# Performance work log

Measured on AMD Instinct MI355X. Metric: run time of the kernel, lower is better.

Reference implementation:

```python
import jax, jax.numpy as jnp
import numpy as np

HIDDEN = 1024
N_HEADS = 16
HEAD_DIM = HIDDEN // N_HEADS


def apply_rope(x, freqs):
    # x: [b, s, h, d]; freqs: [s, d//2]
    b, s, h, d = x.shape
    x2 = x.reshape(b, s, h, d // 2, 2)
    x_real, x_imag = x2[..., 0], x2[..., 1]
    cos = jnp.cos(freqs)[None, :, None, :]  # [1, s, 1, d//2]
    sin = jnp.sin(freqs)[None, :, None, :]
    out_real = x_real * cos - x_imag * sin
    out_imag = x_real * sin + x_imag * cos
    return jnp.stack([out_real, out_imag], axis=-1).reshape(b, s, h, d)


def setup_inputs() -> dict:
    key = jax.random.key(0)
    k_x, k_f, k_wq, k_bq, k_wo, k_bo = jax.random.split(key, 6)
    b, s = 2, 2048
    x = jax.random.normal(k_x, (b, s, HIDDEN), dtype=jnp.float32)
    freqs = jax.random.normal(k_f, (s, HEAD_DIM // 2), dtype=jnp.float32)
    lim = 1.0 / np.sqrt(HIDDEN)
    W_qkv = jax.random.uniform(k_wq, (HIDDEN, 3 * HIDDEN), jnp.float32, -lim, lim)
    b_qkv = jax.random.uniform(k_bq, (3 * HIDDEN,), jnp.float32, -lim, lim)
    W_out = jax.random.uniform(k_wo, (HIDDEN, HIDDEN), jnp.float32, -lim, lim)
    b_out = jax.random.uniform(k_bo, (HIDDEN,), jnp.float32, -lim, lim)
    return {"x": x, "freqs": freqs, "W_qkv": W_qkv, "b_qkv": b_qkv,
            "W_out": W_out, "b_out": b_out}


def reference(x, freqs, W_qkv, b_qkv, W_out, b_out):
    b, s, c = x.shape
    h, d = N_HEADS, HEAD_DIM
    qkv = jnp.einsum('bsc,cf->bsf', x, W_qkv) + b_qkv  # [b, s, 3*c]
    qkv = qkv.reshape(b, s, 3, h, d)
    q, k, v = qkv[:, :, 0], qkv[:, :, 1], qkv[:, :, 2]  # [b, s, h, d]
    q = apply_rope(q, freqs)
    k = apply_rope(k, freqs)
    scale = 1.0 / np.sqrt(d).astype(np.float32)
    scores = jnp.einsum('bqhd,bkhd->bhqk', q, k) * scale  # [b, h, s, s]
    attn = jax.nn.softmax(scores, axis=-1)
    out = jnp.einsum('bhqk,bkhd->bqhd', attn, v).reshape(b, s, c)
    return jnp.einsum('bsc,cf->bsf', out, W_out) + b_out
```

## Files before the change

### kernel.cpp

```cpp
#include <hip/hip_runtime.h>
#include <math.h>

constexpr int kB = 2;
constexpr int kS = 2048;
constexpr int kC = 1024;
constexpr int kH = 16;
constexpr int kD = 64;
constexpr int kF = 3072;
constexpr int kT = kB * kS;

typedef __attribute__((ext_vector_type(8))) short short8v;
typedef __attribute__((ext_vector_type(4))) short short4v;
typedef __attribute__((ext_vector_type(4))) float f32x4;
typedef __attribute__((ext_vector_type(16))) float f32x16;

__device__ __forceinline__ short f2bf(float f) {
    unsigned u = __builtin_bit_cast(unsigned, f);
    u += 0x7fffu + ((u >> 16) & 1u);
    return (short)(u >> 16);
}

__device__ __forceinline__ unsigned cvtpk(float a, float b) {
    unsigned r;
    asm("v_cvt_pk_bf16_f32 %0, %1, %2" : "=v"(r) : "v"(a), "v"(b));
    return r;
}

__device__ __forceinline__ void plane32_swap(unsigned& a, unsigned& b) {
    asm volatile("v_permlane32_swap_b32 %0, %1" : "+v"(a), "+v"(b));
}

__device__ __forceinline__ unsigned pk_bf16(float a, float b) {
    unsigned ua = __builtin_bit_cast(unsigned, a);
    ua += 0x7fffu + ((ua >> 16) & 1u);
    unsigned ub = __builtin_bit_cast(unsigned, b);
    ub += 0x7fffu + ((ub >> 16) & 1u);
    return (ua >> 16) | (ub & 0xffff0000u);
}

__device__ __forceinline__ void gl_lds16(const void* g, void* l) {
    __builtin_amdgcn_global_load_lds(
        (const __attribute__((address_space(1))) char*)g,
        (__attribute__((address_space(3))) char*)l, 16, 0, 0);
}

__device__ __forceinline__ f32x4 mfma16(short8v a, short8v b, f32x4 c) {
    return __builtin_amdgcn_mfma_f32_16x16x32_bf16(a, b, c, 0, 0, 0);
}
__device__ __forceinline__ f32x16 mfma32(short8v a, short8v b, f32x16 c) {
    return __builtin_amdgcn_mfma_f32_32x32x16_bf16(a, b, c, 0, 0, 0);
}

__device__ __forceinline__ void tcvt_body(const float* __restrict__ w,
                                          short* __restrict__ wt, int K, int N,
                                          int bx, int by, int t, float Ts[64][65]) {
    const int n0 = bx * 64, k0 = by * 64;
    const int r = t >> 4, c4 = (t & 15) * 4;
#pragma unroll
    for (int rr = 0; rr < 64; rr += 16) {
        float4 v = *reinterpret_cast<const float4*>(&w[(size_t)(k0 + r + rr) * N + n0 + c4]);
        Ts[r + rr][c4 + 0] = v.x; Ts[r + rr][c4 + 1] = v.y;
        Ts[r + rr][c4 + 2] = v.z; Ts[r + rr][c4 + 3] = v.w;
    }
    __syncthreads();
#pragma unroll
    for (int rr = 0; rr < 64; rr += 16) {
        int n = r + rr;
        short4v o = { f2bf(Ts[c4 + 0][n]), f2bf(Ts[c4 + 1][n]),
                      f2bf(Ts[c4 + 2][n]), f2bf(Ts[c4 + 3][n]) };
        *reinterpret_cast<short4v*>(&wt[(size_t)(n0 + n) * K + k0 + c4]) = o;
    }
}

__global__ __launch_bounds__(256) void prep_kernel(
    const float* __restrict__ x, short* __restrict__ xb,
    const float* __restrict__ wq, short* __restrict__ wqt,
    const float* __restrict__ wo, short* __restrict__ wot,
    const float* __restrict__ freqs, float* __restrict__ cost,
    float* __restrict__ sint) {
    __shared__ float Ts[64][65];
    const int bid = blockIdx.x, t = threadIdx.x;
    if (bid < 4096) {
        int i = bid * 256 + t;
        float4 v = reinterpret_cast<const float4*>(x)[i];
        short4v o = { f2bf(v.x), f2bf(v.y), f2bf(v.z), f2bf(v.w) };
        reinterpret_cast<short4v*>(xb)[i] = o;
    } else if (bid < 4864) {
        int i = bid - 4096;
        tcvt_body(wq, wqt, kC, kF, i % 48, i / 48, t, Ts);
    } else if (bid < 5120) {
        int i = bid - 4864;
        tcvt_body(wo, wot, kC, kC, i % 16, i / 16, t, Ts);
    } else {
        int i = (bid - 5120) * 256 + t;
        float f = freqs[i];
        float s, c;
        sincosf(f, &s, &c);
        cost[i] = c; sint[i] = s;
    }
}

__device__ __forceinline__ void gemm_main(const short* __restrict__ A,
                                          const short* __restrict__ Bt,
                                          int m0, int n0, short* Als, short* Bls,
                                          f32x4 acc[4][4]) {
    const int tid = threadIdx.x, wid = tid >> 6, lane = tid & 63;
    const int srow = lane >> 3, schunk = lane & 7;
    const int fr = lane & 15, fg = lane >> 4;
    const int wm = (wid >> 1) * 64, wn = (wid & 1) * 64;
    for (int kt = 0; kt < 1024; kt += 64) {
        __syncthreads();
#pragma unroll
        for (int j = 0; j < 4; ++j) {
            int i = wid * 4 + j;
            int row = i * 8 + srow;
            gl_lds16(&A[(size_t)(m0 + row) * 1024 + kt + ((schunk ^ (row & 7)) << 3)],
                     &Als[i * 512]);
        }
#pragma unroll
        for (int j = 0; j < 4; ++j) {
            int i = wid * 4 + j;
            int row = i * 8 + srow;
            gl_lds16(&Bt[(size_t)(n0 + row) * 1024 + kt + ((schunk ^ (row & 7)) << 3)],
                     &Bls[i * 512]);
        }
        __syncthreads();
#pragma unroll
        for (int kk = 0; kk < 2; ++kk) {
            short8v af[4], bf[4];
#pragma unroll
            for (int fm = 0; fm < 4; ++fm) {
                int row = wm + fm * 16 + fr;
                af[fm] = *reinterpret_cast<const short8v*>(
                    &Als[row * 64 + (((fg + 4 * kk) ^ (row & 7)) << 3)]);
            }
#pragma unroll
            for (int fn = 0; fn < 4; ++fn) {
                int row = wn + fn * 16 + fr;
                bf[fn] = *reinterpret_cast<const short8v*>(
                    &Bls[row * 64 + (((fg + 4 * kk) ^ (row & 7)) << 3)]);
            }
#pragma unroll
            for (int fm = 0; fm < 4; ++fm)
#pragma unroll
                for (int fn = 0; fn < 4; ++fn)
                    acc[fm][fn] = mfma16(af[fm], bf[fn], acc[fm][fn]);
        }
    }
}

__global__ __launch_bounds__(256) void qkv_gemm_kernel(
    const short* __restrict__ xb, const short* __restrict__ wqt,
    const float* __restrict__ bias, const float* __restrict__ cost,
    const float* __restrict__ sint,
    short* __restrict__ qg, short* __restrict__ kg, short* __restrict__ vt) {
    __shared__ __attribute__((aligned(16))) short Als[128 * 64];
    __shared__ __attribute__((aligned(16))) short Bls[128 * 64];
    f32x4 acc[4][4] = {};
    const int tid = threadIdx.x, wid = tid >> 6, lane = tid & 63;
    const int m0 = blockIdx.y * 128, n0 = blockIdx.x * 128;
    gemm_main(xb, wqt, m0, n0, Als, Bls, acc);

    const int fr = lane & 15, fg = lane >> 4;
    const int wm = (wid >> 1) * 64, wn = (wid & 1) * 64;
    const int which = (n0 + wn) >> 10;
    const int bidx = m0 >> 11;
#pragma unroll
    for (int fn = 0; fn < 4; ++fn) {
        int col = n0 + wn + fn * 16 + fr;
        float bv = bias[col];
        int d = col & 63;
        int h = (col >> 6) & 15;
        int p0 = d >> 1;
        int odd = d & 1;
#pragma unroll
        for (int fm = 0; fm < 4; ++fm) {
            int r0 = m0 + wm + fm * 16 + fg * 4;
            int s0 = r0 & 2047;
            float c[4];
#pragma unroll
            for (int r = 0; r < 4; ++r) c[r] = acc[fm][fn][r] + bv;
            if (which < 2) {
#pragma unroll
                for (int r = 0; r < 4; ++r) {
                    float cs = cost[(s0 + r) * 32 + p0];
                    float sn = sint[(s0 + r) * 32 + p0];
                    float p = __shfl_xor(c[r], 1);
                    float o = odd ? fmaf(p, sn, c[r] * cs) : fmaf(-p, sn, c[r] * cs);
                    c[r] = (which == 0) ? o * 0.1803368801f : o;
                }
                short* dst = which ? kg : qg;
                size_t base = ((size_t)(bidx * 16 + h) * 2048 + s0) * 64 + d;
#pragma unroll
                for (int r = 0; r < 4; ++r) dst[base + (size_t)r * 64] = f2bf(c[r]);
            } else {
                short4v o = { f2bf(c[0]), f2bf(c[1]), f2bf(c[2]), f2bf(c[3]) };
                *reinterpret_cast<short4v*>(
                    &vt[((size_t)(bidx * 16 + h) * 64 + d) * 2048 + s0]) = o;
            }
        }
    }
}

__global__ __launch_bounds__(256, 3) void attn_mfma_kernel(
    const short* __restrict__ qg, const short* __restrict__ kg,
    const short* __restrict__ vt, short* __restrict__ ab) {
    __shared__ __attribute__((aligned(16))) short LDSBUF[16384];
    short* Kls = LDSBUF;
    short* Vls = LDSBUF + 8192;
    const int tid = threadIdx.x, wid = tid >> 6, lane = tid & 63;
    const int l31 = lane & 31, hi = lane >> 5;
    const int r8 = lane >> 3, c8 = lane & 7;

    const int bid = blockIdx.x;
    const int swz = (bid & 7) * 128 + (bid >> 3);
    const int bh = swz >> 5;
    const int q0 = (swz & 31) * 64;

    const short* qb = qg + (size_t)bh * 2048 * 64;
    const short* kb = kg + (size_t)bh * 2048 * 64;
    const short* vb = vt + (size_t)bh * 64 * 2048;

    short8v qf[2][4];
#pragma unroll
    for (int qt = 0; qt < 2; ++qt)
#pragma unroll
        for (int kkq = 0; kkq < 4; ++kkq)
            qf[qt][kkq] = *reinterpret_cast<const short8v*>(
                &qb[(size_t)(q0 + qt * 32 + l31) * 64 + kkq * 16 + hi * 8]);

    f32x16 o[2][2] = {};
    float l_loc[2] = {0.f, 0.f};

    const int soffK = 8 * (c8 ^ r8);

    for (int t = 0; t < 16; ++t) {
        const int kt = t * 128;
        __syncthreads();
#pragma unroll
        for (int j = 0; j < 4; ++j)
            gl_lds16(kb + (size_t)(kt + wid * 32 + j * 8 + r8) * 64 + soffK,
                     Kls + (wid * 32 + j * 8) * 64);
#pragma unroll
        for (int j = 0; j < 4; ++j) {
            int d = wid * 16 + j * 4 + (lane >> 4);
            int c = lane & 15;
            gl_lds16(vb + (size_t)d * 2048 + kt + ((c ^ (d & 15)) * 8),
                     Vls + (wid * 16 + j * 4) * 128);
        }
        __syncthreads();

        f32x16 sacc[2] = {};
#pragma unroll
        for (int kkq = 0; kkq < 4; ++kkq) {
            short8v kf = *reinterpret_cast<const short8v*>(
                &Kls[(wid * 32 + l31) * 64 + (((kkq * 2 + hi) ^ (l31 & 7)) << 3)]);
            sacc[0] = mfma32(kf, qf[0][kkq], sacc[0]);
            sacc[1] = mfma32(kf, qf[1][kkq], sacc[1]);
        }

        short8v pb[2][2];
#pragma unroll
        for (int qt = 0; qt < 2; ++qt) {
#pragma unroll
            for (int r = 0; r < 16; ++r)
                sacc[qt][r] = __builtin_amdgcn_exp2f(sacc[qt][r]);
            float t8[8];
#pragma unroll
            for (int r = 0; r < 8; ++r) t8[r] = sacc[qt][r] + sacc[qt][r + 8];
            float t4[4];
#pragma unroll
            for (int r = 0; r < 4; ++r) t4[r] = t8[r] + t8[r + 4];
            l_loc[qt] += (t4[0] + t4[1]) + (t4[2] + t4[3]);
            unsigned c[4][2];
#pragma unroll
            for (int g = 0; g < 4; ++g) {
                c[g][0] = cvtpk(sacc[qt][g * 4 + 0], sacc[qt][g * 4 + 1]);
                c[g][1] = cvtpk(sacc[qt][g * 4 + 2], sacc[qt][g * 4 + 3]);
            }
#pragma unroll
            for (int kk = 0; kk < 2; ++kk) {
                unsigned x0 = c[2 * kk][0], y0 = c[2 * kk + 1][0];
                unsigned x1 = c[2 * kk][1], y1 = c[2 * kk + 1][1];
                plane32_swap(x0, y0);
                plane32_swap(x1, y1);
                uint4 w;
                w.x = x0; w.y = x1; w.z = y0; w.w = y1;
                pb[qt][kk] = __builtin_bit_cast(short8v, w);
            }
        }

#pragma unroll
        for (int kk = 0; kk < 2; ++kk)
#pragma unroll
            for (int fd = 0; fd < 2; ++fd) {
                int d = fd * 32 + l31;
                short8v vf = *reinterpret_cast<const short8v*>(
                    &Vls[d * 128 + (((wid * 4 + kk * 2 + hi) ^ (d & 15)) << 3)]);
                o[fd][0] = mfma32(vf, pb[0][kk], o[fd][0]);
                o[fd][1] = mfma32(vf, pb[1][kk], o[fd][1]);
            }
    }

    __syncthreads();

    float* Oacc = reinterpret_cast<float*>(LDSBUF);
    float* lacc = Oacc + 64 * 65;
    float l2[2];
#pragma unroll
    for (int qt = 0; qt < 2; ++qt)
        l2[qt] = l_loc[qt] + __shfl_xor(l_loc[qt], 32);
    for (int w = 0; w < 4; ++w) {
        if (wid == w) {
#pragma unroll
            for (int qt = 0; qt < 2; ++qt) {
                int q = qt * 32 + l31;
#pragma unroll
                for (int fd = 0; fd < 2; ++fd)
#pragma unroll
                    for (int r = 0; r < 16; ++r) {
                        int d = fd * 32 + (r & 3) + 8 * (r >> 2) + 4 * hi;
                        if (w == 0) Oacc[q * 65 + d] = o[fd][qt][r];
                        else        Oacc[q * 65 + d] += o[fd][qt][r];
                    }
                if (hi == 0) {
                    if (w == 0) lacc[q] = l2[qt];
                    else        lacc[q] += l2[qt];
                }
            }
        }
        __syncthreads();
    }
    {
        const int q = tid >> 2, dc = (tid & 3) * 16;
        const float inv = 1.f / lacc[q];
        unsigned u[8];
#pragma unroll
        for (int i = 0; i < 8; ++i) {
            float a = Oacc[q * 65 + dc + 2 * i] * inv;
            float b = Oacc[q * 65 + dc + 2 * i + 1] * inv;
            u[i] = pk_bf16(a, b);
        }
        const int bb = bh >> 4, hh = bh & 15;
        size_t base = (size_t)(bb * 2048 + q0 + q) * 1024 + hh * 64 + dc;
        uint4 w0; w0.x = u[0]; w0.y = u[1]; w0.z = u[2]; w0.w = u[3];
        uint4 w1; w1.x = u[4]; w1.y = u[5]; w1.z = u[6]; w1.w = u[7];
        *reinterpret_cast<uint4*>(&ab[base]) = w0;
        *reinterpret_cast<uint4*>(&ab[base + 8]) = w1;
    }
}

__global__ __launch_bounds__(256) void out_gemm_kernel(
    const short* __restrict__ ab, const short* __restrict__ wot,
    const float* __restrict__ bias, float* __restrict__ out) {
    __shared__ __attribute__((aligned(16))) short Als[128 * 64];
    __shared__ __attribute__((aligned(16))) short Bls[128 * 64];
    f32x4 acc[4][4] = {};
    const int tid = threadIdx.x, wid = tid >> 6, lane = tid & 63;
    const int m0 = blockIdx.y * 128, n0 = blockIdx.x * 128;
    gemm_main(ab, wot, m0, n0, Als, Bls, acc);
    const int fr = lane & 15, fg = lane >> 4;
    const int wm = (wid >> 1) * 64, wn = (wid & 1) * 64;
#pragma unroll
    for (int fn = 0; fn < 4; ++fn) {
        int col = n0 + wn + fn * 16 + fr;
        float bv = bias[col];
#pragma unroll
        for (int fm = 0; fm < 4; ++fm) {
            int r0 = m0 + wm + fm * 16 + fg * 4;
#pragma unroll
            for (int r = 0; r < 4; ++r)
                out[(size_t)(r0 + r) * 1024 + col] = acc[fm][fn][r] + bv;
        }
    }
}

extern "C" void kernel_launch(void* const* d_in, const int* in_sizes, int n_in,
                              void* d_out, int out_size, void* d_ws, size_t ws_size,
                              hipStream_t stream) {
    const float* x     = (const float*)d_in[0];
    const float* freqs = (const float*)d_in[1];
    const float* W_qkv = (const float*)d_in[2];
    const float* b_qkv = (const float*)d_in[3];
    const float* W_out = (const float*)d_in[4];
    const float* b_out = (const float*)d_in[5];
    float* out = (float*)d_out;

    char* w = (char*)d_ws;
    short* xb  = (short*)w;  w += (size_t)kT * kC * 2;
    short* wqt = (short*)w;  w += (size_t)kF * kC * 2;
    short* wot = (short*)w;  w += (size_t)kC * kC * 2;
    short* qgw = (short*)w;  w += (size_t)kB * kH * kS * kD * 2;
    short* kgw = (short*)w;  w += (size_t)kB * kH * kS * kD * 2;
    short* vtw = (short*)w;  w += (size_t)kB * kH * kS * kD * 2;
    short* abw = (short*)w;  w += (size_t)kT * kC * 2;
    float* costt = (float*)w; w += (size_t)kS * (kD / 2) * 4;
    float* sintt = (float*)w; w += (size_t)kS * (kD / 2) * 4;

    prep_kernel<<<dim3(5376), 256, 0, stream>>>(x, xb, W_qkv, wqt, W_out, wot,
                                                freqs, costt, sintt);
    qkv_gemm_kernel<<<dim3(kF / 128, kT / 128), 256, 0, stream>>>(
        xb, wqt, b_qkv, costt, sintt, qgw, kgw, vtw);
    attn_mfma_kernel<<<dim3(1024), 256, 0, stream>>>(qgw, kgw, vtw, abw);
    out_gemm_kernel<<<dim3(kC / 128, kT / 128), 256, 0, stream>>>(abw, wot, b_out, out);
}
```

Baseline: 135.5 us.

## Load K/V fragments directly from global memory instead of staging through LDS

The attention kernel no longer stages K and V tiles into shared memory with global-to-LDS copies and two barriers per iteration. Each wave now reads its own K rows and V^T columns straight from global memory into registers before the MFMAs. This removes the per-tile __syncthreads and the LDS traffic, and shrinks shared memory to only the final reduction buffer. It also drops the occupancy hint from launch bounds. The cost is that global loads now sit in the critical path without explicit prefetch, and register pressure goes up.

```diff
diff --git a/kernel.cpp b/kernel.cpp
--- a/kernel.cpp
+++ b/kernel.cpp
@@ -202,15 +202,12 @@
     }
 }
 
-__global__ __launch_bounds__(256, 3) void attn_mfma_kernel(
+__global__ __launch_bounds__(256) void attn_mfma_kernel(
     const short* __restrict__ qg, const short* __restrict__ kg,
     const short* __restrict__ vt, short* __restrict__ ab) {
-    __shared__ __attribute__((aligned(16))) short LDSBUF[16384];
-    short* Kls = LDSBUF;
-    short* Vls = LDSBUF + 8192;
+    __shared__ float Oacc[64 * 65 + 64];
     const int tid = threadIdx.x, wid = tid >> 6, lane = tid & 63;
     const int l31 = lane & 31, hi = lane >> 5;
-    const int r8 = lane >> 3, c8 = lane & 7;
 
     const int bid = blockIdx.x;
     const int swz = (bid & 7) * 128 + (bid >> 3);
@@ -232,31 +229,26 @@
     f32x16 o[2][2] = {};
     float l_loc[2] = {0.f, 0.f};
 
-    const int soffK = 8 * (c8 ^ r8);
+    const short* Krow = kb + (size_t)(wid * 32 + l31) * 64 + hi * 8;
+    const short* V0 = vb + (size_t)l31 * 2048 + wid * 32 + hi * 8;
+    const short* V1 = vb + (size_t)(32 + l31) * 2048 + wid * 32 + hi * 8;
 
     for (int t = 0; t < 16; ++t) {
-        const int kt = t * 128;
-        __syncthreads();
-#pragma unroll
-        for (int j = 0; j < 4; ++j)
-            gl_lds16(kb + (size_t)(kt + wid * 32 + j * 8 + r8) * 64 + soffK,
-                     Kls + (wid * 32 + j * 8) * 64);
-#pragma unroll
-        for (int j = 0; j < 4; ++j) {
-            int d = wid * 16 + j * 4 + (lane >> 4);
-            int c = lane & 15;
-            gl_lds16(vb + (size_t)d * 2048 + kt + ((c ^ (d & 15)) * 8),
-                     Vls + (wid * 16 + j * 4) * 128);
-        }
-        __syncthreads();
-
         f32x16 sacc[2] = {};
+        short8v kf[4];
+#pragma unroll
+        for (int kkq = 0; kkq < 4; ++kkq)
+            kf[kkq] = *reinterpret_cast<const short8v*>(Krow + kkq * 16);
+        short8v vf[2][2];
+#pragma unroll
+        for (int kk = 0; kk < 2; ++kk) {
+            vf[kk][0] = *reinterpret_cast<const short8v*>(V0 + kk * 16);
+            vf[kk][1] = *reinterpret_cast<const short8v*>(V1 + kk * 16);
+        }
 #pragma unroll
         for (int kkq = 0; kkq < 4; ++kkq) {
-            short8v kf = *reinterpret_cast<const short8v*>(
-                &Kls[(wid * 32 + l31) * 64 + (((kkq * 2 + hi) ^ (l31 & 7)) << 3)]);
-            sacc[0] = mfma32(kf, qf[0][kkq], sacc[0]);
-            sacc[1] = mfma32(kf, qf[1][kkq], sacc[1]);
+            sacc[0] = mfma32(kf[kkq], qf[0][kkq], sacc[0]);
+            sacc[1] = mfma32(kf[kkq], qf[1][kkq], sacc[1]);
         }
 
         short8v pb[2][2];
@@ -291,20 +283,20 @@
         }
 
 #pragma unroll
-        for (int kk = 0; kk < 2; ++kk)
-#pragma unroll
-            for (int fd = 0; fd < 2; ++fd) {
-                int d = fd * 32 + l31;
-                short8v vf = *reinterpret_cast<const short8v*>(
-                    &Vls[d * 128 + (((wid * 4 + kk * 2 + hi) ^ (d & 15)) << 3)]);
-                o[fd][0] = mfma32(vf, pb[0][kk], o[fd][0]);
-                o[fd][1] = mfma32(vf, pb[1][kk], o[fd][1]);
-            }
+        for (int kk = 0; kk < 2; ++kk) {
+            o[0][0] = mfma32(vf[kk][0], pb[0][kk], o[0][0]);
+            o[0][1] = mfma32(vf[kk][0], pb[1][kk], o[0][1]);
+            o[1][0] = mfma32(vf[kk][1], pb[0][kk], o[1][0]);
+            o[1][1] = mfma32(vf[kk][1], pb[1][kk], o[1][1]);
+        }
+
+        Krow += 128 * 64;
+        V0 += 128;
+        V1 += 128;
     }
 
     __syncthreads();
 
-    float* Oacc = reinterpret_cast<float*>(LDSBUF);
     float* lacc = Oacc + 64 * 65;
     float l2[2];
 #pragma unroll
```

New measurement: 147.7 us. 9.0% more time.

## Shrink output GEMM tile to 128x64 and raise attention occupancy bound

Applied to the files above, without the earlier changes.

The output projection GEMM moves from 128x128 tiles to 128x64 tiles with its own inlined main loop. This doubles the grid from 256 to 512 blocks so the 256 CUs of the device are better filled. The attention kernel's launch bound goes from 3 to 4 blocks per CU, which pressures the compiler to use fewer registers and may cause spills. Smaller GEMM tiles mean less reuse of the A operand per load.

```diff
diff --git a/kernel.cpp b/kernel.cpp
--- a/kernel.cpp
+++ b/kernel.cpp
@@ -202,7 +202,7 @@
     }
 }
 
-__global__ __launch_bounds__(256, 3) void attn_mfma_kernel(
+__global__ __launch_bounds__(256, 4) void attn_mfma_kernel(
     const short* __restrict__ qg, const short* __restrict__ kg,
     const short* __restrict__ vt, short* __restrict__ ab) {
     __shared__ __attribute__((aligned(16))) short LDSBUF[16384];
@@ -354,15 +354,55 @@
     const short* __restrict__ ab, const short* __restrict__ wot,
     const float* __restrict__ bias, float* __restrict__ out) {
     __shared__ __attribute__((aligned(16))) short Als[128 * 64];
-    __shared__ __attribute__((aligned(16))) short Bls[128 * 64];
-    f32x4 acc[4][4] = {};
+    __shared__ __attribute__((aligned(16))) short Bls[64 * 64];
+    f32x4 acc[4][2] = {};
     const int tid = threadIdx.x, wid = tid >> 6, lane = tid & 63;
-    const int m0 = blockIdx.y * 128, n0 = blockIdx.x * 128;
-    gemm_main(ab, wot, m0, n0, Als, Bls, acc);
+    const int srow = lane >> 3, schunk = lane & 7;
     const int fr = lane & 15, fg = lane >> 4;
-    const int wm = (wid >> 1) * 64, wn = (wid & 1) * 64;
-#pragma unroll
-    for (int fn = 0; fn < 4; ++fn) {
+    const int wm = (wid >> 1) * 64, wn = (wid & 1) * 32;
+    const int m0 = blockIdx.y * 128, n0 = blockIdx.x * 64;
+
+    for (int kt = 0; kt < 1024; kt += 64) {
+        __syncthreads();
+#pragma unroll
+        for (int j = 0; j < 4; ++j) {
+            int i = wid * 4 + j;
+            int row = i * 8 + srow;
+            gl_lds16(&ab[(size_t)(m0 + row) * 1024 + kt + ((schunk ^ (row & 7)) << 3)],
+                     &Als[i * 512]);
+        }
+#pragma unroll
+        for (int j = 0; j < 2; ++j) {
+            int i = wid * 2 + j;
+            int row = i * 8 + srow;
+            gl_lds16(&wot[(size_t)(n0 + row) * 1024 + kt + ((schunk ^ (row & 7)) << 3)],
+                     &Bls[i * 512]);
+        }
+        __syncthreads();
+#pragma unroll
+        for (int kk = 0; kk < 2; ++kk) {
+            short8v af[4], bf[2];
+#pragma unroll
+            for (int fm = 0; fm < 4; ++fm) {
+                int row = wm + fm * 16 + fr;
+                af[fm] = *reinterpret_cast<const short8v*>(
+                    &Als[row * 64 + (((fg + 4 * kk) ^ (row & 7)) << 3)]);
+            }
+#pragma unroll
+            for (int fn = 0; fn < 2; ++fn) {
+                int row = wn + fn * 16 + fr;
+                bf[fn] = *reinterpret_cast<const short8v*>(
+                    &Bls[row * 64 + (((fg + 4 * kk) ^ (row & 7)) << 3)]);
+            }
+#pragma unroll
+            for (int fm = 0; fm < 4; ++fm)
+#pragma unroll
+                for (int fn = 0; fn < 2; ++fn)
+                    acc[fm][fn] = mfma16(af[fm], bf[fn], acc[fm][fn]);
+        }
+    }
+#pragma unroll
+    for (int fn = 0; fn < 2; ++fn) {
         int col = n0 + wn + fn * 16 + fr;
         float bv = bias[col];
 #pragma unroll
@@ -402,5 +442,5 @@
     qkv_gemm_kernel<<<dim3(kF / 128, kT / 128), 256, 0, stream>>>(
         xb, wqt, b_qkv, costt, sintt, qgw, kgw, vtw);
     attn_mfma_kernel<<<dim3(1024), 256, 0, stream>>>(qgw, kgw, vtw, abw);
-    out_gemm_kernel<<<dim3(kC / 128, kT / 128), 256, 0, stream>>>(abw, wot, b_out, out);
-}
+    out_gemm_kernel<<<dim3(kC / 64, kT / 128), 256, 0, stream>>>(abw, wot, b_out, out);
+}
```

After: 176.1 us. 30.0% more time.
